# Kernel optimization log

Measured on AMD Instinct MI355X. Metric: run time of the kernel, lower is better.

Reference implementation:

```python
import jax, jax.numpy as jnp
import numpy as np

TEMPERATURE = 0.1
EPS = 1e-8  # torch F.cosine_similarity eps


def setup_inputs() -> dict:
    key = jax.random.key(0)
    k1, k2, k3 = jax.random.split(key, 3)
    N, M, D = 1024, 65536, 128
    return {
        "image_real_features": jax.random.normal(k1, (N, D), dtype=jnp.float32),
        "image_perturbed_features": jax.random.normal(k2, (N, D), dtype=jnp.float32),
        "memory_bank_features": jax.random.normal(k3, (M, D), dtype=jnp.float32),
    }


def _safe_norm(x, axis=-1):
    # matches torch cosine_similarity's clamp_min(eps) on the norms
    return jnp.maximum(jnp.linalg.norm(x, axis=axis), EPS)


def reference(image_real_features, image_perturbed_features, memory_bank_features):
    real_norm = _safe_norm(image_real_features)          # [N]
    pert_norm = _safe_norm(image_perturbed_features)     # [N]
    mem_norm = _safe_norm(memory_bank_features)          # [M]

    # positive cosine similarity, per-sample
    pos = jnp.sum(image_real_features * image_perturbed_features, axis=-1)
    pos = pos / (real_norm * pert_norm) / TEMPERATURE    # [N]

    # negatives: normalize once + GEMM instead of broadcast O(N*M*D)
    real_n = image_real_features / real_norm[:, None]    # [N, D]
    mem_n = memory_bank_features / mem_norm[:, None]     # [M, D]
    neg = jnp.einsum("nd,md->nm", real_n, mem_n) / TEMPERATURE  # [N, M]
    neg = jnp.sum(neg, axis=1)                           # [N]

    logits = jnp.stack([pos, neg], axis=-1)              # [N, 2]
    # labels are all zeros -> CE = -log_softmax(logits)[:, 0]
    loss = -jax.nn.log_softmax(logits, axis=-1)[:, 0]
    return jnp.mean(loss)  # CrossEntropyLoss(mean) then mean of scalar: same
```

## Files before the change

### kernel.cpp

```cpp
#include <hip/hip_runtime.h>
#include <math.h>

#define TEMP_INV 10.0f
#define EPSN 1e-8f
#define NPART 256

__device__ __forceinline__ float inv_norm(float ss) {
    float x = fmaxf(ss, EPSN * EPSN);
    float y = rsqrtf(x);
    return y * (1.5f - 0.5f * x * y * y);
}

__device__ __forceinline__ void wave_sum4(float& v0, float& v1, float& v2, float& v3) {
    #pragma unroll
    for (int off = 32; off > 0; off >>= 1) {
        v0 += __shfl_xor(v0, off, 64);
        v1 += __shfl_xor(v1, off, 64);
        v2 += __shfl_xor(v2, off, 64);
        v3 += __shfl_xor(v3, off, 64);
    }
}

__global__ __launch_bounds__(1024) void k_memsum(const float4* __restrict__ mem4,
                                                 float* __restrict__ P,
                                                 float* __restrict__ out, int M) {
    const int tid  = threadIdx.x;
    if (blockIdx.x == 0 && tid == 0) out[0] = 0.0f;

    const int lane = tid & 63;
    const int w    = tid >> 6;
    const int half = lane >> 5;
    const int sl   = lane & 31;
    const int gw   = blockIdx.x * 16 + w;
    const int GW   = gridDim.x * 16;
    const int P2   = M >> 1;

    float a0 = 0.f, a1 = 0.f, a2 = 0.f, a3 = 0.f;

    int p = gw;
    if (P2 == GW * 8) {
        float4 v[8];
        #pragma unroll
        for (int k = 0; k < 8; ++k)
            v[k] = mem4[(size_t)(2 * (gw + k * GW) + half) * 32 + sl];
        #pragma unroll
        for (int k = 0; k < 8; ++k) {
            float ss = v[k].x * v[k].x + v[k].y * v[k].y
                     + v[k].z * v[k].z + v[k].w * v[k].w;
            #pragma unroll
            for (int off = 16; off > 0; off >>= 1)
                ss += __shfl_xor(ss, off, 64);
            float inv = inv_norm(ss);
            a0 += v[k].x * inv; a1 += v[k].y * inv;
            a2 += v[k].z * inv; a3 += v[k].w * inv;
        }
        p = P2;
    }
    for (; p < P2; p += GW) {
        float4 v = mem4[(size_t)(2 * p + half) * 32 + sl];
        float ss = v.x * v.x + v.y * v.y + v.z * v.z + v.w * v.w;
        #pragma unroll
        for (int off = 16; off > 0; off >>= 1)
            ss += __shfl_xor(ss, off, 64);
        float inv = inv_norm(ss);
        a0 += v.x * inv; a1 += v.y * inv; a2 += v.z * inv; a3 += v.w * inv;
    }
    if ((M & 1) && gw == 0 && half == 0) {
        float4 v = mem4[(size_t)(M - 1) * 32 + sl];
        float ss = v.x * v.x + v.y * v.y + v.z * v.z + v.w * v.w;
        #pragma unroll
        for (int off = 16; off > 0; off >>= 1)
            ss += __shfl_xor(ss, off, 64);
        float inv = inv_norm(ss);
        a0 += v.x * inv; a1 += v.y * inv; a2 += v.z * inv; a3 += v.w * inv;
    }

    __shared__ float sacc[16][2][128];
    ((float4*)sacc[w][half])[sl] = make_float4(a0, a1, a2, a3);
    __syncthreads();
    if (tid < 128) {
        float s = 0.f;
        #pragma unroll
        for (int i = 0; i < 16; ++i)
            s += sacc[i][0][tid] + sacc[i][1][tid];
        P[blockIdx.x * 128 + tid] = s;
    }
}

__global__ __launch_bounds__(1024) void k_loss(const float2* __restrict__ real,
                                               const float2* __restrict__ pert,
                                               const float* __restrict__ P,
                                               float* __restrict__ out,
                                               int N, float invN) {
    __shared__ float red[8][128];
    __shared__ float s[128];
    const int t = threadIdx.x;
    {
        const int d = t & 127;
        const int g = t >> 7;
        float acc = 0.f;
        #pragma unroll
        for (int j = 0; j < 32; ++j)
            acc += P[(g * 32 + j) * 128 + d];
        red[g][d] = acc;
    }
    __syncthreads();
    if (t < 128) {
        float v = 0.f;
        #pragma unroll
        for (int i = 0; i < 8; ++i) v += red[i][t];
        s[t] = v;
    }
    __syncthreads();

    const int lane = t & 63;
    const int w    = t >> 6;
    const int gw   = blockIdx.x * 16 + w;
    const int GW   = gridDim.x * 16;
    const float2 sv = make_float2(s[2 * lane], s[2 * lane + 1]);

    float lsum = 0.f;
    for (int n = gw; n < N; n += GW) {
        float2 r = real[n * 64 + lane];
        float2 p = pert[n * 64 + lane];
        float ssr = r.x * r.x + r.y * r.y;
        float ssp = p.x * p.x + p.y * p.y;
        float drp = r.x * p.x + r.y * p.y;
        float drs = r.x * sv.x + r.y * sv.y;
        wave_sum4(ssr, ssp, drp, drs);
        float inr = inv_norm(ssr);
        float inp = inv_norm(ssp);
        float pos = drp * inr * inp * TEMP_INV;
        float neg = drs * inr * TEMP_INV;
        float mx  = fmaxf(pos, neg);
        float lse = mx + __logf(__expf(pos - mx) + __expf(neg - mx));
        lsum += lse - pos;
    }

    __shared__ float wl[16];
    if (lane == 0) wl[w] = lsum;
    __syncthreads();
    if (t == 0) {
        float v = 0.f;
        #pragma unroll
        for (int i = 0; i < 16; ++i) v += wl[i];
        atomicAdd(out, v * invN);
    }
}

extern "C" void kernel_launch(void* const* d_in, const int* in_sizes, int n_in,
                              void* d_out, int out_size, void* d_ws, size_t ws_size,
                              hipStream_t stream) {
    const float* real = (const float*)d_in[0];
    const float* pert = (const float*)d_in[1];
    const float* memb = (const float*)d_in[2];
    float* out = (float*)d_out;

    const int D = 128;
    const int N = in_sizes[0] / D;
    const int M = in_sizes[2] / D;

    float* P = (float*)d_ws;

    k_memsum<<<NPART, 1024, 0, stream>>>((const float4*)memb, P, out, M);
    k_loss<<<32, 1024, 0, stream>>>((const float2*)real, (const float2*)pert,
                                    P, out, N, 1.0f / (float)N);
}
```

Measured before the change: 83.74 us.

## Fuse memsum and loss kernels via atomic counter grid barrier

Merges the two kernels into one launch. The first 32 blocks spin on an atomic counter until all 256 partial-sum blocks have finished, then compute the loss, which removes the gap between the two kernel launches. The load loop is also restructured to keep 4 loads in flight and issue the rest inside the compute loop, lowering register pressure. In exchange it adds a memset launch for the counter and relies on all 256 blocks being co-resident so the spin cannot deadlock.

```diff
diff --git a/kernel.cpp b/kernel.cpp
--- a/kernel.cpp
+++ b/kernel.cpp
@@ -4,6 +4,7 @@
 #define TEMP_INV 10.0f
 #define EPSN 1e-8f
 #define NPART 256
+#define LOSS_BLOCKS 32
 
 __device__ __forceinline__ float inv_norm(float ss) {
     float x = fmaxf(ss, EPSN * EPSN);
@@ -21,10 +22,15 @@
     }
 }
 
-__global__ __launch_bounds__(1024) void k_memsum(const float4* __restrict__ mem4,
-                                                 float* __restrict__ P,
-                                                 float* __restrict__ out, int M) {
-    const int tid  = threadIdx.x;
+__global__ __launch_bounds__(1024, 8) void k_fused(
+        const float4*  __restrict__ mem4,
+        const float2*  __restrict__ real,
+        const float2*  __restrict__ pert,
+        float*         __restrict__ P,
+        unsigned int*  __restrict__ counter,
+        float*         __restrict__ out,
+        int M, int N, float invN) {
+    const int tid = threadIdx.x;
     if (blockIdx.x == 0 && tid == 0) out[0] = 0.0f;
 
     const int lane = tid & 63;
@@ -41,10 +47,12 @@
     if (P2 == GW * 8) {
         float4 v[8];
         #pragma unroll
-        for (int k = 0; k < 8; ++k)
+        for (int k = 0; k < 4; ++k)
             v[k] = mem4[(size_t)(2 * (gw + k * GW) + half) * 32 + sl];
         #pragma unroll
         for (int k = 0; k < 8; ++k) {
+            if (k + 4 < 8)
+                v[k + 4] = mem4[(size_t)(2 * (gw + (k + 4) * GW) + half) * 32 + sl];
             float ss = v[k].x * v[k].x + v[k].y * v[k].y
                      + v[k].z * v[k].z + v[k].w * v[k].w;
             #pragma unroll
@@ -85,19 +93,26 @@
             s += sacc[i][0][tid] + sacc[i][1][tid];
         P[blockIdx.x * 128 + tid] = s;
     }
-}
 
-__global__ __launch_bounds__(1024) void k_loss(const float2* __restrict__ real,
-                                               const float2* __restrict__ pert,
-                                               const float* __restrict__ P,
-                                               float* __restrict__ out,
-                                               int N, float invN) {
+    __threadfence();
+    __syncthreads();
+    if (tid == 0)
+        __hip_atomic_fetch_add(counter, 1u, __ATOMIC_RELEASE,
+                               __HIP_MEMORY_SCOPE_AGENT);
+    if (blockIdx.x >= LOSS_BLOCKS) return;
+    if (tid == 0) {
+        while (__hip_atomic_load(counter, __ATOMIC_ACQUIRE,
+                                 __HIP_MEMORY_SCOPE_AGENT) < (unsigned)NPART)
+            __builtin_amdgcn_s_sleep(8);
+    }
+    __syncthreads();
+    __threadfence();
+
     __shared__ float red[8][128];
-    __shared__ float s[128];
-    const int t = threadIdx.x;
+    __shared__ float ssum[128];
     {
-        const int d = t & 127;
-        const int g = t >> 7;
+        const int d = tid & 127;
+        const int g = tid >> 7;
         float acc = 0.f;
         #pragma unroll
         for (int j = 0; j < 32; ++j)
@@ -105,27 +120,25 @@
         red[g][d] = acc;
     }
     __syncthreads();
-    if (t < 128) {
+    if (tid < 128) {
         float v = 0.f;
         #pragma unroll
-        for (int i = 0; i < 8; ++i) v += red[i][t];
-        s[t] = v;
+        for (int i = 0; i < 8; ++i) v += red[i][tid];
+        ssum[tid] = v;
     }
     __syncthreads();
 
-    const int lane = t & 63;
-    const int w    = t >> 6;
-    const int gw   = blockIdx.x * 16 + w;
-    const int GW   = gridDim.x * 16;
-    const float2 sv = make_float2(s[2 * lane], s[2 * lane + 1]);
+    const int gw2 = blockIdx.x * 16 + w;
+    const int GW2 = LOSS_BLOCKS * 16;
+    const float2 sv = make_float2(ssum[2 * lane], ssum[2 * lane + 1]);
 
     float lsum = 0.f;
-    for (int n = gw; n < N; n += GW) {
+    for (int n = gw2; n < N; n += GW2) {
         float2 r = real[n * 64 + lane];
-        float2 p = pert[n * 64 + lane];
+        float2 q = pert[n * 64 + lane];
         float ssr = r.x * r.x + r.y * r.y;
-        float ssp = p.x * p.x + p.y * p.y;
-        float drp = r.x * p.x + r.y * p.y;
+        float ssp = q.x * q.x + q.y * q.y;
+        float drp = r.x * q.x + r.y * q.y;
         float drs = r.x * sv.x + r.y * sv.y;
         wave_sum4(ssr, ssp, drp, drs);
         float inr = inv_norm(ssr);
@@ -140,7 +153,7 @@
     __shared__ float wl[16];
     if (lane == 0) wl[w] = lsum;
     __syncthreads();
-    if (t == 0) {
+    if (tid == 0) {
         float v = 0.f;
         #pragma unroll
         for (int i = 0; i < 16; ++i) v += wl[i];
@@ -161,8 +174,12 @@
     const int M = in_sizes[2] / D;
 
     float* P = (float*)d_ws;
+    unsigned int* counter =
+        (unsigned int*)((char*)d_ws + (size_t)NPART * 128 * sizeof(float));
 
-    k_memsum<<<NPART, 1024, 0, stream>>>((const float4*)memb, P, out, M);
-    k_loss<<<32, 1024, 0, stream>>>((const float2*)real, (const float2*)pert,
-                                    P, out, N, 1.0f / (float)N);
+    hipMemsetAsync(counter, 0, sizeof(unsigned int), stream);
+
+    k_fused<<<NPART, 1024, 0, stream>>>((const float4*)memb,
+                                        (const float2*)real, (const float2*)pert,
+                                        P, counter, out, M, N, 1.0f / (float)N);
 }
```

Result: slower. 154.4 us (+84.4%).
